# Performance work log

Measured on AMD Instinct MI355X. Metric: run time of the kernel, lower is better.

Reference implementation:

```python
import jax, jax.numpy as jnp
import numpy as np

N, IN_FEATURES, OUT_FEATURES = 1048576, 32, 128


def setup_inputs() -> dict:
    key = jax.random.key(0)
    kx, kc = jax.random.split(key)
    x = jax.random.normal(kx, (N, IN_FEATURES), dtype=jnp.float32)
    # nn.init.normal_(centres, 0, 1); nn.init.constant_(log_sigmas, 0)
    centres = jax.random.normal(kc, (OUT_FEATURES, IN_FEATURES), dtype=jnp.float32)
    log_sigmas = jnp.zeros((OUT_FEATURES,), dtype=jnp.float32)
    return {"x": x, "centres": centres, "log_sigmas": log_sigmas}


def reference(x, centres, log_sigmas):
    x2 = jnp.sum(x * x, axis=-1, keepdims=True)            # (N, 1)
    c2 = jnp.sum(centres * centres, axis=-1)               # (out,)
    cross = jnp.einsum('ni,oi->no', x, centres)            # (N, out) GEMM
    sqdist = jnp.maximum(x2 - 2.0 * cross + c2, 0.0)       # clamp fp round-off
    # original: exp(-(sqrt(sqdist)/sigma)^2) == exp(-sqdist / sigma^2)
    inv_var = jnp.exp(-2.0 * log_sigmas)                   # (out,)
    return jnp.exp(-sqdist * inv_var)                      # (N, out)
```

## Files before the change

### kernel.cpp

```cpp
#include <hip/hip_runtime.h>

constexpr int IN_F  = 32;
constexpr int OUT_F = 128;
constexpr int BLOCK = 256;
constexpr int WAVES = BLOCK / 64;
constexpr int RSTAGE = 8;

using f32x2 = __attribute__((ext_vector_type(2))) float;

__global__ __launch_bounds__(BLOCK)
void rbf_kernel(const float* __restrict__ x,
                const float* __restrict__ centres,
                const float* __restrict__ log_sigmas,
                float* __restrict__ out,
                int rows_per_wave)
{
    __shared__ float4 xs[WAVES][RSTAGE][IN_F / 4];
    __shared__ float  x2s[WAVES][RSTAGE];

    const int tid  = threadIdx.x;
    const int wv   = tid >> 6;
    const int lane = tid & 63;

    const int o0 = lane * 2;
    float c0[IN_F], c1[IN_F];
    float c2a = 0.f, c2b = 0.f;
    #pragma unroll
    for (int kc = 0; kc < IN_F / 4; ++kc) {
        const float4 a = *reinterpret_cast<const float4*>(centres + (size_t)(o0 + 0) * IN_F + kc * 4);
        const float4 b = *reinterpret_cast<const float4*>(centres + (size_t)(o0 + 1) * IN_F + kc * 4);
        c0[kc*4+0] = a.x; c0[kc*4+1] = a.y; c0[kc*4+2] = a.z; c0[kc*4+3] = a.w;
        c1[kc*4+0] = b.x; c1[kc*4+1] = b.y; c1[kc*4+2] = b.z; c1[kc*4+3] = b.w;
        c2a = fmaf(a.x,a.x,c2a); c2a = fmaf(a.y,a.y,c2a);
        c2a = fmaf(a.z,a.z,c2a); c2a = fmaf(a.w,a.w,c2a);
        c2b = fmaf(b.x,b.x,c2b); c2b = fmaf(b.y,b.y,c2b);
        c2b = fmaf(b.z,b.z,c2b); c2b = fmaf(b.w,b.w,c2b);
    }
    const float iv0 = __expf(-2.0f * log_sigmas[o0 + 0]);
    const float iv1 = __expf(-2.0f * log_sigmas[o0 + 1]);

    const size_t waveRow0 = ((size_t)blockIdx.x * WAVES + wv) * (size_t)rows_per_wave;
    const int rs = lane >> 3;
    const int q  = lane & 7;

    for (int it = 0; it < rows_per_wave; it += RSTAGE) {
        const float4 v = *reinterpret_cast<const float4*>(
            x + (waveRow0 + it) * IN_F + lane * 4);
        float s;
        s = v.x * v.x;
        s = fmaf(v.y, v.y, s);
        s = fmaf(v.z, v.z, s);
        s = fmaf(v.w, v.w, s);
        s += __shfl_xor(s, 1);
        s += __shfl_xor(s, 2);
        s += __shfl_xor(s, 4);
        xs[wv][rs][q] = v;
        if (q == 0) x2s[wv][rs] = s;
        __syncthreads();

        #pragma unroll
        for (int rr = 0; rr < RSTAGE; ++rr) {
            float acc0 = 0.f, acc1 = 0.f;
            #pragma unroll
            for (int kc = 0; kc < IN_F / 4; ++kc) {
                const float4 xk = xs[wv][rr][kc];
                acc0 = fmaf(xk.x, c0[kc*4+0], acc0);
                acc0 = fmaf(xk.y, c0[kc*4+1], acc0);
                acc0 = fmaf(xk.z, c0[kc*4+2], acc0);
                acc0 = fmaf(xk.w, c0[kc*4+3], acc0);
                acc1 = fmaf(xk.x, c1[kc*4+0], acc1);
                acc1 = fmaf(xk.y, c1[kc*4+1], acc1);
                acc1 = fmaf(xk.z, c1[kc*4+2], acc1);
                acc1 = fmaf(xk.w, c1[kc*4+3], acc1);
            }
            const float x2 = x2s[wv][rr];
            const float t0 = fmaxf(fmaf(-2.0f, acc0, x2 + c2a), 0.0f);
            const float t1 = fmaxf(fmaf(-2.0f, acc1, x2 + c2b), 0.0f);
            f32x2 o;
            o.x = __expf(-t0 * iv0);
            o.y = __expf(-t1 * iv1);
            __builtin_nontemporal_store(o,
                reinterpret_cast<f32x2*>(out + (waveRow0 + it + rr) * OUT_F + o0));
        }
        __syncthreads();
    }
}

extern "C" void kernel_launch(void* const* d_in, const int* in_sizes, int n_in,
                              void* d_out, int out_size, void* d_ws, size_t ws_size,
                              hipStream_t stream) {
    const float* x          = (const float*)d_in[0];
    const float* centres    = (const float*)d_in[1];
    const float* log_sigmas = (const float*)d_in[2];
    float* out = (float*)d_out;

    const int n = in_sizes[0] / IN_F;
    const int blocks = 2048;
    const int rows_per_block = n / blocks;
    const int rows_per_wave  = rows_per_block / WAVES;
    rbf_kernel<<<blocks, BLOCK, 0, stream>>>(x, centres, log_sigmas, out, rows_per_wave);
}
```

Measured before the change: 154.3 us.

## Prefetch next x tile into registers, double-buffer LDS, drop block barriers

Each wave now handles 16 rows per stage. It loads the next tile's x into registers while computing the current one, and alternates between two per-wave LDS buffers. The block-wide __syncthreads calls are replaced by an lgkmcnt wait, since each wave only reads its own LDS slice. The x-squared norms now reach lanes by shuffle instead of through shared memory, and launch bounds ask for 4 blocks per CU. The goal is to hide global load latency and remove cross-wave barrier stalls, at the cost of more registers and a wave-local synchronisation scheme that depends on hardware ordering.

```diff
diff --git a/kernel.cpp b/kernel.cpp
--- a/kernel.cpp
+++ b/kernel.cpp
@@ -1,22 +1,21 @@
 #include <hip/hip_runtime.h>
 
-constexpr int IN_F  = 32;
-constexpr int OUT_F = 128;
-constexpr int BLOCK = 256;
-constexpr int WAVES = BLOCK / 64;
-constexpr int RSTAGE = 8;
+constexpr int IN_F   = 32;
+constexpr int OUT_F  = 128;
+constexpr int BLOCK  = 256;
+constexpr int WAVES  = BLOCK / 64;
+constexpr int RSTAGE = 16;
 
 using f32x2 = __attribute__((ext_vector_type(2))) float;
 
-__global__ __launch_bounds__(BLOCK)
+__global__ __launch_bounds__(BLOCK, 4)
 void rbf_kernel(const float* __restrict__ x,
                 const float* __restrict__ centres,
                 const float* __restrict__ log_sigmas,
                 float* __restrict__ out,
                 int rows_per_wave)
 {
-    __shared__ float4 xs[WAVES][RSTAGE][IN_F / 4];
-    __shared__ float  x2s[WAVES][RSTAGE];
+    __shared__ float4 xs[WAVES][2][RSTAGE][IN_F / 4];
 
     const int tid  = threadIdx.x;
     const int wv   = tid >> 6;
@@ -40,30 +39,39 @@
     const float iv1 = __expf(-2.0f * log_sigmas[o0 + 1]);
 
     const size_t waveRow0 = ((size_t)blockIdx.x * WAVES + wv) * (size_t)rows_per_wave;
+    const float* xbase = x + waveRow0 * IN_F;
     const int rs = lane >> 3;
     const int q  = lane & 7;
 
+    float4 va = *reinterpret_cast<const float4*>(xbase + lane * 4);
+    float4 vb = *reinterpret_cast<const float4*>(xbase + 8 * IN_F + lane * 4);
+
+    int buf = 0;
     for (int it = 0; it < rows_per_wave; it += RSTAGE) {
-        const float4 v = *reinterpret_cast<const float4*>(
-            x + (waveRow0 + it) * IN_F + lane * 4);
-        float s;
-        s = v.x * v.x;
-        s = fmaf(v.y, v.y, s);
-        s = fmaf(v.z, v.z, s);
-        s = fmaf(v.w, v.w, s);
-        s += __shfl_xor(s, 1);
-        s += __shfl_xor(s, 2);
-        s += __shfl_xor(s, 4);
-        xs[wv][rs][q] = v;
-        if (q == 0) x2s[wv][rs] = s;
-        __syncthreads();
+        float sa = va.x * va.x;
+        sa = fmaf(va.y, va.y, sa); sa = fmaf(va.z, va.z, sa); sa = fmaf(va.w, va.w, sa);
+        sa += __shfl_xor(sa, 1); sa += __shfl_xor(sa, 2); sa += __shfl_xor(sa, 4);
+        float sb = vb.x * vb.x;
+        sb = fmaf(vb.y, vb.y, sb); sb = fmaf(vb.z, vb.z, sb); sb = fmaf(vb.w, vb.w, sb);
+        sb += __shfl_xor(sb, 1); sb += __shfl_xor(sb, 2); sb += __shfl_xor(sb, 4);
+
+        xs[wv][buf][rs][q]     = va;
+        xs[wv][buf][8 + rs][q] = vb;
+
+        if (it + RSTAGE < rows_per_wave) {
+            const float* nxt = xbase + (size_t)(it + RSTAGE) * IN_F;
+            va = *reinterpret_cast<const float4*>(nxt + lane * 4);
+            vb = *reinterpret_cast<const float4*>(nxt + 8 * IN_F + lane * 4);
+        }
+
+        asm volatile("s_waitcnt lgkmcnt(0)" ::: "memory");
 
         #pragma unroll
         for (int rr = 0; rr < RSTAGE; ++rr) {
             float acc0 = 0.f, acc1 = 0.f;
             #pragma unroll
             for (int kc = 0; kc < IN_F / 4; ++kc) {
-                const float4 xk = xs[wv][rr][kc];
+                const float4 xk = xs[wv][buf][rr][kc];
                 acc0 = fmaf(xk.x, c0[kc*4+0], acc0);
                 acc0 = fmaf(xk.y, c0[kc*4+1], acc0);
                 acc0 = fmaf(xk.z, c0[kc*4+2], acc0);
@@ -73,7 +81,7 @@
                 acc1 = fmaf(xk.z, c1[kc*4+2], acc1);
                 acc1 = fmaf(xk.w, c1[kc*4+3], acc1);
             }
-            const float x2 = x2s[wv][rr];
+            const float x2 = (rr < 8) ? __shfl(sa, rr * 8) : __shfl(sb, (rr - 8) * 8);
             const float t0 = fmaxf(fmaf(-2.0f, acc0, x2 + c2a), 0.0f);
             const float t1 = fmaxf(fmaf(-2.0f, acc1, x2 + c2b), 0.0f);
             f32x2 o;
@@ -82,7 +90,7 @@
             __builtin_nontemporal_store(o,
                 reinterpret_cast<f32x2*>(out + (waveRow0 + it + rr) * OUT_F + o0));
         }
-        __syncthreads();
+        buf ^= 1;
     }
 }
 
```

After: 158.9 us. +3.0%, slower.

## Load x rows via scalar s_load into SGPRs, double-buffered, dropping LDS staging

Applied to the files above, without the earlier changes.

Each wave now reads whole input rows with s_load_dwordx16 into scalar registers, double-buffered across two rows, instead of staging through LDS with block-wide barriers. The row norm is computed per lane from the broadcast row, the FMAs use packed f32x2 math, the grid doubles to 4096 blocks, and launch bounds request occupancy of 4. The aim is to remove LDS traffic and __syncthreads stalls so the kernel is bound only by the output write. In exchange it relies on inline asm and SGPR pressure, and scalar loads go through the small scalar cache.

```diff
diff --git a/kernel.cpp b/kernel.cpp
--- a/kernel.cpp
+++ b/kernel.cpp
@@ -4,33 +4,83 @@
 constexpr int OUT_F = 128;
 constexpr int BLOCK = 256;
 constexpr int WAVES = BLOCK / 64;
-constexpr int RSTAGE = 8;
 
-using f32x2 = __attribute__((ext_vector_type(2))) float;
+using f32x2  = __attribute__((ext_vector_type(2)))  float;
+using f32x16 = __attribute__((ext_vector_type(16))) float;
 
-__global__ __launch_bounds__(BLOCK)
+__device__ __forceinline__ const float* uniform_ptr(const float* p) {
+    const uint64_t u = reinterpret_cast<uint64_t>(p);
+    const uint32_t lo = __builtin_amdgcn_readfirstlane((uint32_t)u);
+    const uint32_t hi = __builtin_amdgcn_readfirstlane((uint32_t)(u >> 32));
+    return reinterpret_cast<const float*>(((uint64_t)hi << 32) | lo);
+}
+
+__device__ __forceinline__ void sload_row(const float* p, f32x16& lo, f32x16& hi) {
+    const float* up = uniform_ptr(p);
+    asm volatile("s_load_dwordx16 %0, %2, 0x0\n\t"
+                 "s_load_dwordx16 %1, %2, 0x40"
+                 : "=&s"(lo), "=&s"(hi)
+                 : "s"(up));
+}
+
+__device__ __forceinline__ void wait_smem() {
+    asm volatile("s_waitcnt lgkmcnt(0)" ::: "memory");
+    __builtin_amdgcn_sched_barrier(0);
+}
+
+__device__ __forceinline__ void compute_row(const f32x16& lo, const f32x16& hi,
+                                            const f32x2* c0p, const f32x2* c1p,
+                                            float c2a, float c2b, float iv0, float iv1,
+                                            float* orow, int o0)
+{
+    f32x2 a0 = {0.f, 0.f}, a1 = {0.f, 0.f}, s2 = {0.f, 0.f};
+    #pragma unroll
+    for (int j = 0; j < 8; ++j) {
+        const f32x2 xp = { lo[2*j], lo[2*j+1] };
+        a0 = __builtin_elementwise_fma(xp, c0p[j], a0);
+        a1 = __builtin_elementwise_fma(xp, c1p[j], a1);
+        s2 = __builtin_elementwise_fma(xp, xp, s2);
+    }
+    #pragma unroll
+    for (int j = 0; j < 8; ++j) {
+        const f32x2 xp = { hi[2*j], hi[2*j+1] };
+        a0 = __builtin_elementwise_fma(xp, c0p[8+j], a0);
+        a1 = __builtin_elementwise_fma(xp, c1p[8+j], a1);
+        s2 = __builtin_elementwise_fma(xp, xp, s2);
+    }
+    const float x2   = s2.x + s2.y;
+    const float acc0 = a0.x + a0.y;
+    const float acc1 = a1.x + a1.y;
+    const float t0 = fmaxf(fmaf(-2.0f, acc0, x2 + c2a), 0.0f);
+    const float t1 = fmaxf(fmaf(-2.0f, acc1, x2 + c2b), 0.0f);
+    f32x2 o;
+    o.x = __expf(-t0 * iv0);
+    o.y = __expf(-t1 * iv1);
+    __builtin_nontemporal_store(o, reinterpret_cast<f32x2*>(orow + o0));
+}
+
+__global__ __launch_bounds__(BLOCK, 4)
 void rbf_kernel(const float* __restrict__ x,
                 const float* __restrict__ centres,
                 const float* __restrict__ log_sigmas,
                 float* __restrict__ out,
                 int rows_per_wave)
 {
-    __shared__ float4 xs[WAVES][RSTAGE][IN_F / 4];
-    __shared__ float  x2s[WAVES][RSTAGE];
-
     const int tid  = threadIdx.x;
     const int wv   = tid >> 6;
     const int lane = tid & 63;
 
     const int o0 = lane * 2;
-    float c0[IN_F], c1[IN_F];
+    f32x2 c0p[IN_F / 2], c1p[IN_F / 2];
     float c2a = 0.f, c2b = 0.f;
     #pragma unroll
     for (int kc = 0; kc < IN_F / 4; ++kc) {
         const float4 a = *reinterpret_cast<const float4*>(centres + (size_t)(o0 + 0) * IN_F + kc * 4);
         const float4 b = *reinterpret_cast<const float4*>(centres + (size_t)(o0 + 1) * IN_F + kc * 4);
-        c0[kc*4+0] = a.x; c0[kc*4+1] = a.y; c0[kc*4+2] = a.z; c0[kc*4+3] = a.w;
-        c1[kc*4+0] = b.x; c1[kc*4+1] = b.y; c1[kc*4+2] = b.z; c1[kc*4+3] = b.w;
+        c0p[2*kc + 0] = (f32x2){a.x, a.y};
+        c0p[2*kc + 1] = (f32x2){a.z, a.w};
+        c1p[2*kc + 0] = (f32x2){b.x, b.y};
+        c1p[2*kc + 1] = (f32x2){b.z, b.w};
         c2a = fmaf(a.x,a.x,c2a); c2a = fmaf(a.y,a.y,c2a);
         c2a = fmaf(a.z,a.z,c2a); c2a = fmaf(a.w,a.w,c2a);
         c2b = fmaf(b.x,b.x,c2b); c2b = fmaf(b.y,b.y,c2b);
@@ -40,49 +90,26 @@
     const float iv1 = __expf(-2.0f * log_sigmas[o0 + 1]);
 
     const size_t waveRow0 = ((size_t)blockIdx.x * WAVES + wv) * (size_t)rows_per_wave;
-    const int rs = lane >> 3;
-    const int q  = lane & 7;
+    const float* p    = x   + waveRow0 * IN_F;
+    float*       orow = out + waveRow0 * OUT_F;
 
-    for (int it = 0; it < rows_per_wave; it += RSTAGE) {
-        const float4 v = *reinterpret_cast<const float4*>(
-            x + (waveRow0 + it) * IN_F + lane * 4);
-        float s;
-        s = v.x * v.x;
-        s = fmaf(v.y, v.y, s);
-        s = fmaf(v.z, v.z, s);
-        s = fmaf(v.w, v.w, s);
-        s += __shfl_xor(s, 1);
-        s += __shfl_xor(s, 2);
-        s += __shfl_xor(s, 4);
-        xs[wv][rs][q] = v;
-        if (q == 0) x2s[wv][rs] = s;
-        __syncthreads();
+    f32x16 alo, ahi, blo, bhi;
 
-        #pragma unroll
-        for (int rr = 0; rr < RSTAGE; ++rr) {
-            float acc0 = 0.f, acc1 = 0.f;
-            #pragma unroll
-            for (int kc = 0; kc < IN_F / 4; ++kc) {
-                const float4 xk = xs[wv][rr][kc];
-                acc0 = fmaf(xk.x, c0[kc*4+0], acc0);
-                acc0 = fmaf(xk.y, c0[kc*4+1], acc0);
-                acc0 = fmaf(xk.z, c0[kc*4+2], acc0);
-                acc0 = fmaf(xk.w, c0[kc*4+3], acc0);
-                acc1 = fmaf(xk.x, c1[kc*4+0], acc1);
-                acc1 = fmaf(xk.y, c1[kc*4+1], acc1);
-                acc1 = fmaf(xk.z, c1[kc*4+2], acc1);
-                acc1 = fmaf(xk.w, c1[kc*4+3], acc1);
-            }
-            const float x2 = x2s[wv][rr];
-            const float t0 = fmaxf(fmaf(-2.0f, acc0, x2 + c2a), 0.0f);
-            const float t1 = fmaxf(fmaf(-2.0f, acc1, x2 + c2b), 0.0f);
-            f32x2 o;
-            o.x = __expf(-t0 * iv0);
-            o.y = __expf(-t1 * iv1);
-            __builtin_nontemporal_store(o,
-                reinterpret_cast<f32x2*>(out + (waveRow0 + it + rr) * OUT_F + o0));
-        }
-        __syncthreads();
+    sload_row(p, alo, ahi);
+    wait_smem();
+
+    for (int r = 0; r < rows_per_wave; r += 2) {
+        sload_row(p + IN_F, blo, bhi);
+        compute_row(alo, ahi, c0p, c1p, c2a, c2b, iv0, iv1, orow, o0);
+        wait_smem();
+
+        const float* pn = (r + 2 < rows_per_wave) ? (p + 2 * IN_F) : p;
+        sload_row(pn, alo, ahi);
+        compute_row(blo, bhi, c0p, c1p, c2a, c2b, iv0, iv1, orow + OUT_F, o0);
+        wait_smem();
+
+        p    += 2 * IN_F;
+        orow += 2 * OUT_F;
     }
 }
 
@@ -95,8 +122,7 @@
     float* out = (float*)d_out;
 
     const int n = in_sizes[0] / IN_F;
-    const int blocks = 2048;
-    const int rows_per_block = n / blocks;
-    const int rows_per_wave  = rows_per_block / WAVES;
+    const int blocks = 4096;
+    const int rows_per_wave = n / (blocks * WAVES);
     rbf_kernel<<<blocks, BLOCK, 0, stream>>>(x, centres, log_sigmas, out, rows_per_wave);
 }
```

Result: slower. 169.6 us (+9.9%).
